# Optimization experiments

Hardware: AMD Instinct MI355X
Metric: run time of the kernel (lower is better)

## Reference

```python
import jax, jax.numpy as jnp
import numpy as np

B, T, E, H = 32, 2048, 512, 512


def setup_inputs() -> dict:
    key = jax.random.key(0)
    k1, k2, k3 = jax.random.split(key, 3)
    scale_w = 1.0 / np.sqrt(E)
    scale_u = 1.0 / np.sqrt(H)
    return {
        "src_seq": jax.random.normal(k1, (B, T, E), dtype=jnp.float32),
        "W": jax.random.normal(k2, (E, 4 * H), dtype=jnp.float32) * scale_w,
        "U": jax.random.normal(k3, (H, 4 * H), dtype=jnp.float32) * scale_u,
        "b": jnp.zeros((4 * H,), dtype=jnp.float32),
        "h0": jnp.zeros((B, H), dtype=jnp.float32),
        "c0": jnp.zeros((B, H), dtype=jnp.float32),
    }


def reference(src_seq, W, U, b, h0, c0):
    """LSTM encoder: scan an LSTMCell over time.

    Returns (output, encoding_hidden_states [T,B,H], final_state), where
    output == final hidden state, matching the original forward().
    """

    def step(carry, x_t):
        h, c = carry
        # Fused gate pre-activations: [B, 4H], keras LSTMCell order i,f,g,o
        z = x_t @ W + h @ U + b
        i, f, g, o = jnp.split(z, 4, axis=-1)
        i = jax.nn.sigmoid(i)
        f = jax.nn.sigmoid(f)
        g = jnp.tanh(g)
        o = jax.nn.sigmoid(o)
        c_new = f * c + i * g
        h_new = o * jnp.tanh(c_new)
        return (h_new, c_new), h_new

    xs = jnp.swapaxes(src_seq, 0, 1)  # [T, B, E]
    (h_T, c_T), hs = jax.lax.scan(step, (h0, c0), xs)
    # (output, list-of-per-step hidden states stacked, final hidden state)
    return h_T, hs, h_T
```

## Files before the change

kernel.cpp:

```cpp
#include <hip/hip_runtime.h>
#include <stdint.h>

#define T_STEPS 2048
#define BATCH 32
#define EDIM 512
#define HDIM 512

typedef __attribute__((ext_vector_type(8))) short bf16x8;
typedef __attribute__((ext_vector_type(4))) float f32x4;
typedef unsigned long long u64t;

#define FIXED_WS 0x831000ull

__device__ inline unsigned short f2bf(float x){
    unsigned u = __float_as_uint(x);
    unsigned r = (u + 0x7fffu + ((u >> 16) & 1u)) >> 16;
    return (unsigned short)r;
}
__device__ inline float bf2f(unsigned short s){
    return __uint_as_float(((unsigned)s) << 16);
}
__device__ inline float sigmoid_f(float x){
    return __builtin_amdgcn_rcpf(1.f + __expf(-x));
}
__device__ inline float tanh_f(float x){
    float xc = fminf(30.f, fmaxf(-30.f, x));
    float e = __expf(2.f * xc);
    return (e - 1.f) * __builtin_amdgcn_rcpf(e + 1.f);
}

__global__ void prep_kernel(const float* __restrict__ W, const float* __restrict__ U,
                            const float* __restrict__ h0,
                            unsigned short* __restrict__ Wh, unsigned short* __restrict__ Wl,
                            unsigned short* __restrict__ Uh, unsigned short* __restrict__ Ul,
                            unsigned* __restrict__ hbuf){
    int idx = blockIdx.x * blockDim.x + threadIdx.x;
    int stride = gridDim.x * blockDim.x;
    const int total = 2 * EDIM * 2048;
    for (int i = idx; i < total; i += stride){
        int mat = i >> 20;
        int r = i & 1048575;
        int k = r >> 11;
        int col = r & 2047;
        float v = (mat ? U : W)[(size_t)k * 2048 + col];
        unsigned short hi = f2bf(v);
        unsigned short lo = f2bf(v - bf2f(hi));
        int cg = (col & 511) >> 4;
        int hc = col & 15;
        int g  = col >> 9;
        int kb = k >> 5;
        int kgrp = (k >> 3) & 3;
        int j = k & 7;
        size_t dst = (size_t)cg * 32768 + (size_t)kb * 2048 + (size_t)g * 512
                   + (size_t)(kgrp * 16 + hc) * 8 + j;
        if (mat){ Uh[dst] = hi; Ul[dst] = lo; } else { Wh[dst] = hi; Wl[dst] = lo; }
    }
    for (int i = idx; i < BATCH * HDIM; i += stride){
        float v = h0[i];
        unsigned short hi = f2bf(v);
        unsigned short lo = f2bf(v - bf2f(hi));
        hbuf[i] = (unsigned)hi | ((unsigned)lo << 16);
    }
}

__global__ __launch_bounds__(256) void xw_gemm_chunk(
        const float* __restrict__ src,
        const unsigned short* __restrict__ Wh, const unsigned short* __restrict__ Wl,
        float* __restrict__ xWc, int t0){
    const int bid = blockIdx.x;
    const int mtile = bid >> 5;
    const int cg = bid & 31;
    const int tid = threadIdx.x;
    const int lane = tid & 63;
    const int w = tid >> 6;
    const int tc = mtile * 4 + w;
    const int t = t0 + tc;
    const int lc = lane & 15;
    const int kgrp = lane >> 4;

    const uint4* WhF = reinterpret_cast<const uint4*>(Wh) + (size_t)cg * 4096;
    const uint4* WlF = reinterpret_cast<const uint4*>(Wl) + (size_t)cg * 4096;

    f32x4 acc[2][4];
    #pragma unroll
    for (int bt = 0; bt < 2; bt++)
        #pragma unroll
        for (int ct = 0; ct < 4; ct++)
            #pragma unroll
            for (int r = 0; r < 4; r++) acc[bt][ct][r] = 0.f;

    for (int kb = 0; kb < 16; kb++){
        bf16x8 ah[2], al[2];
        #pragma unroll
        for (int bt = 0; bt < 2; bt++){
            const float* xp = src + ((size_t)(bt * 16 + lc) * 2048 + t) * 512 + kb * 32 + kgrp * 8;
            float xv[8];
            *reinterpret_cast<float4*>(&xv[0]) = *reinterpret_cast<const float4*>(xp);
            *reinterpret_cast<float4*>(&xv[4]) = *reinterpret_cast<const float4*>(xp + 4);
            #pragma unroll
            for (int j = 0; j < 8; j++){
                unsigned short hi = f2bf(xv[j]);
                ah[bt][j] = (short)hi;
                al[bt][j] = (short)f2bf(xv[j] - bf2f(hi));
            }
        }
        #pragma unroll
        for (int ct = 0; ct < 4; ct++){
            uint4 bh4 = WhF[kb * 256 + ct * 64 + lane];
            uint4 bl4 = WlF[kb * 256 + ct * 64 + lane];
            bf16x8 bh = *reinterpret_cast<bf16x8*>(&bh4);
            bf16x8 bl = *reinterpret_cast<bf16x8*>(&bl4);
            #pragma unroll
            for (int bt = 0; bt < 2; bt++){
                acc[bt][ct] = __builtin_amdgcn_mfma_f32_16x16x32_bf16(ah[bt], bh, acc[bt][ct], 0, 0, 0);
                acc[bt][ct] = __builtin_amdgcn_mfma_f32_16x16x32_bf16(ah[bt], bl, acc[bt][ct], 0, 0, 0);
                acc[bt][ct] = __builtin_amdgcn_mfma_f32_16x16x32_bf16(al[bt], bh, acc[bt][ct], 0, 0, 0);
            }
        }
    }
    #pragma unroll
    for (int bt = 0; bt < 2; bt++)
        #pragma unroll
        for (int ct = 0; ct < 4; ct++)
            #pragma unroll
            for (int r = 0; r < 4; r++){
                int row_b = bt * 16 + kgrp * 4 + r;
                xWc[((size_t)tc * 32 + row_b) * 2048 + ct * 512 + cg * 16 + lc] = acc[bt][ct][r];
            }
}

__global__ __launch_bounds__(512, 1) void lstm_scan_fast(
        const float* __restrict__ bias, const float* __restrict__ c0,
        const unsigned short* __restrict__ Uh, const unsigned short* __restrict__ Ul,
        unsigned* __restrict__ hbuf, unsigned* __restrict__ done,
        const float* __restrict__ xWc, float* __restrict__ c_ws,
        float* __restrict__ out, int t0, int tlen){
    const int tid  = threadIdx.x;
    const int cg   = blockIdx.x;
    const int lane = tid & 63;
    const int w    = tid >> 6;
    const int bt   = w >> 2;
    const int kq   = w & 3;
    const int lc   = lane & 15;
    const int kgrp = lane >> 4;
    const int row  = bt * 16 + lc;

    __shared__ float z_lds[4][BATCH][65];

    const int cb  = tid >> 4;
    const int chc = tid & 15;
    const int col = cg * 16 + chc;
    float c_state = (t0 == 0) ? c0[(size_t)cb * HDIM + col] : c_ws[(size_t)cb * HDIM + col];
    float bias_g[4];
    #pragma unroll
    for (int g = 0; g < 4; g++) bias_g[g] = bias[g * HDIM + col];

    const uint4* UhF = reinterpret_cast<const uint4*>(Uh) + (size_t)cg * 4096;
    const uint4* UlF = reinterpret_cast<const uint4*>(Ul) + (size_t)cg * 4096;
    bf16x8 ufh[4][4], ufl[4][4];
    #pragma unroll
    for (int i = 0; i < 4; i++){
        int kb = kq * 4 + i;
        #pragma unroll
        for (int ct = 0; ct < 4; ct++){
            uint4 a  = UhF[kb * 256 + ct * 64 + lane];
            uint4 b2 = UlF[kb * 256 + ct * 64 + lane];
            ufh[i][ct] = *reinterpret_cast<bf16x8*>(&a);
            ufl[i][ct] = *reinterpret_cast<bf16x8*>(&b2);
        }
    }

    f32x4 acc[4];
    #pragma unroll
    for (int ct = 0; ct < 4; ct++)
        #pragma unroll
        for (int r = 0; r < 4; r++) acc[ct][r] = 0.f;

    for (int t = t0; t < t0 + tlen; t++){
        const float* xwp = xWc + ((size_t)(t - t0) * 32 + cb) * 2048 + col;
        float zx0 = xwp[0], zx1 = xwp[512], zx2 = xwp[1024], zx3 = xwp[1536];

        if (t > 0){
            const unsigned tgt = (unsigned)t;
            while (true){
                unsigned f = __hip_atomic_load(&done[lane & 31],
                                               __ATOMIC_RELAXED, __HIP_MEMORY_SCOPE_AGENT);
                if (__all(f >= tgt)) break;
                __builtin_amdgcn_s_sleep(1);
            }
        }

        const u64t* hp = reinterpret_cast<const u64t*>(hbuf)
                       + (size_t)(t & 1) * 8192 + (size_t)row * 256;
        u64t hv[16];
        #pragma unroll
        for (int i = 0; i < 4; i++){
            int base = (kq * 4 + i) * 16 + kgrp * 4;
            #pragma unroll
            for (int jp = 0; jp < 4; jp++)
                hv[i * 4 + jp] = __hip_atomic_load(hp + base + jp,
                                                   __ATOMIC_RELAXED, __HIP_MEMORY_SCOPE_AGENT);
        }

        #pragma unroll
        for (int i = 0; i < 4; i++){
            bf16x8 ah, al;
            #pragma unroll
            for (int jp = 0; jp < 4; jp++){
                u64t q = hv[i * 4 + jp];
                unsigned a = (unsigned)q;
                unsigned b = (unsigned)(q >> 32);
                ah[jp * 2    ] = (short)(a & 0xffffu); al[jp * 2    ] = (short)(a >> 16);
                ah[jp * 2 + 1] = (short)(b & 0xffffu); al[jp * 2 + 1] = (short)(b >> 16);
            }
            #pragma unroll
            for (int ct = 0; ct < 4; ct++){
                acc[ct] = __builtin_amdgcn_mfma_f32_16x16x32_bf16(ah, ufh[i][ct], acc[ct], 0, 0, 0);
                acc[ct] = __builtin_amdgcn_mfma_f32_16x16x32_bf16(ah, ufl[i][ct], acc[ct], 0, 0, 0);
                acc[ct] = __builtin_amdgcn_mfma_f32_16x16x32_bf16(al, ufh[i][ct], acc[ct], 0, 0, 0);
            }
        }

        #pragma unroll
        for (int ct = 0; ct < 4; ct++)
            #pragma unroll
            for (int r = 0; r < 4; r++)
                z_lds[kq][bt * 16 + kgrp * 4 + r][ct * 16 + lc] = acc[ct][r];
        __syncthreads();

        float hn;
        {
            float z0 = z_lds[0][cb][chc]      + z_lds[1][cb][chc]      + z_lds[2][cb][chc]      + z_lds[3][cb][chc]      + zx0 + bias_g[0];
            float z1 = z_lds[0][cb][16 + chc] + z_lds[1][cb][16 + chc] + z_lds[2][cb][16 + chc] + z_lds[3][cb][16 + chc] + zx1 + bias_g[1];
            float z2 = z_lds[0][cb][32 + chc] + z_lds[1][cb][32 + chc] + z_lds[2][cb][32 + chc] + z_lds[3][cb][32 + chc] + zx2 + bias_g[2];
            float z3 = z_lds[0][cb][48 + chc] + z_lds[1][cb][48 + chc] + z_lds[2][cb][48 + chc] + z_lds[3][cb][48 + chc] + zx3 + bias_g[3];
            float ig = sigmoid_f(z0);
            float fg = sigmoid_f(z1);
            float gg = tanh_f(z2);
            float og = sigmoid_f(z3);
            float cn = fg * c_state + ig * gg;
            c_state = cn;
            hn = og * tanh_f(cn);
            unsigned short hi = f2bf(hn);
            unsigned short lo = f2bf(hn - bf2f(hi));
            __hip_atomic_store(&hbuf[(size_t)((t + 1) & 1) * (BATCH * HDIM) + (size_t)cb * HDIM + col],
                               (unsigned)hi | ((unsigned)lo << 16),
                               __ATOMIC_RELAXED, __HIP_MEMORY_SCOPE_AGENT);
        }
        __syncthreads();
        if (tid == 0)
            __hip_atomic_store(&done[cg], (unsigned)(t + 1),
                               __ATOMIC_RELAXED, __HIP_MEMORY_SCOPE_AGENT);

        out[16384 + ((size_t)t * BATCH + cb) * HDIM + col] = hn;
        if (t == T_STEPS - 1){
            out[(size_t)cb * HDIM + col] = hn;
            out[16384 + (size_t)T_STEPS * BATCH * HDIM + (size_t)cb * HDIM + col] = hn;
        }

        #pragma unroll
        for (int ct = 0; ct < 4; ct++)
            #pragma unroll
            for (int r = 0; r < 4; r++) acc[ct][r] = 0.f;
    }
    c_ws[(size_t)cb * HDIM + col] = c_state;
}

__global__ __launch_bounds__(512, 2) void lstm_scan_r7(
        const float* __restrict__ src, const float* __restrict__ bias,
        const float* __restrict__ c0,
        const unsigned short* __restrict__ Wh, const unsigned short* __restrict__ Wl,
        const unsigned short* __restrict__ Uh, const unsigned short* __restrict__ Ul,
        unsigned* __restrict__ hbuf, unsigned* __restrict__ cnt,
        float* __restrict__ out){
    const int tid  = threadIdx.x;
    const int cg   = blockIdx.x;
    const int lane = tid & 63;
    const int w    = tid >> 6;
    const int bt   = w >> 2;
    const int kq   = w & 3;
    const int lc   = lane & 15;
    const int kgrp = lane >> 4;
    const int row  = bt * 16 + lc;

    __shared__ float z_lds[4][BATCH][65];

    const int cb  = tid >> 4;
    const int chc = tid & 15;
    const int col = cg * 16 + chc;
    float c_state = c0[(size_t)cb * HDIM + col];
    float bias_g[4];
    #pragma unroll
    for (int g = 0; g < 4; g++) bias_g[g] = bias[g * HDIM + col];

    const uint4* WhF = reinterpret_cast<const uint4*>(Wh) + (size_t)cg * 4096;
    const uint4* WlF = reinterpret_cast<const uint4*>(Wl) + (size_t)cg * 4096;
    const uint4* UhF = reinterpret_cast<const uint4*>(Uh) + (size_t)cg * 4096;
    const uint4* UlF = reinterpret_cast<const uint4*>(Ul) + (size_t)cg * 4096;

    f32x4 acc[4];
    #pragma unroll
    for (int ct = 0; ct < 4; ct++)
        #pragma unroll
        for (int r = 0; r < 4; r++) acc[ct][r] = 0.f;

    auto phaseA = [&](int t){
        #pragma unroll
        for (int i = 0; i < 4; i++){
            int kb = kq * 4 + i;
            const float* xp = src + ((size_t)row * T_STEPS + t) * EDIM + kb * 32 + kgrp * 8;
            float xv[8];
            *reinterpret_cast<float4*>(&xv[0]) = *reinterpret_cast<const float4*>(xp);
            *reinterpret_cast<float4*>(&xv[4]) = *reinterpret_cast<const float4*>(xp + 4);
            bf16x8 ah, al;
            #pragma unroll
            for (int j = 0; j < 8; j++){
                unsigned short hi = f2bf(xv[j]);
                ah[j] = (short)hi;
                al[j] = (short)f2bf(xv[j] - bf2f(hi));
            }
            #pragma unroll
            for (int ct = 0; ct < 4; ct++){
                uint4 bh4 = WhF[kb * 256 + ct * 64 + lane];
                uint4 bl4 = WlF[kb * 256 + ct * 64 + lane];
                bf16x8 bh = *reinterpret_cast<bf16x8*>(&bh4);
                bf16x8 bl = *reinterpret_cast<bf16x8*>(&bl4);
                acc[ct] = __builtin_amdgcn_mfma_f32_16x16x32_bf16(ah, bh, acc[ct], 0, 0, 0);
                acc[ct] = __builtin_amdgcn_mfma_f32_16x16x32_bf16(ah, bl, acc[ct], 0, 0, 0);
                acc[ct] = __builtin_amdgcn_mfma_f32_16x16x32_bf16(al, bh, acc[ct], 0, 0, 0);
            }
        }
    };

    phaseA(0);

    for (int t = 0; t < T_STEPS; t++){
        if (t > 0){
            if (w == 0){
                const unsigned need = 32u * (unsigned)((t + 1) >> 1);
                while (__hip_atomic_load(&cnt[t & 1], __ATOMIC_RELAXED, __HIP_MEMORY_SCOPE_AGENT) < need)
                    __builtin_amdgcn_s_sleep(1);
            }
            __syncthreads();
        }

        const u64t* hp = reinterpret_cast<const u64t*>(hbuf)
                       + (size_t)(t & 1) * 8192 + (size_t)row * 256;
        u64t hv[16];
        #pragma unroll
        for (int i = 0; i < 4; i++){
            int base = (kq * 4 + i) * 16 + kgrp * 4;
            #pragma unroll
            for (int jp = 0; jp < 4; jp++)
                hv[i * 4 + jp] = __hip_atomic_load(hp + base + jp,
                                                   __ATOMIC_RELAXED, __HIP_MEMORY_SCOPE_AGENT);
        }

        #pragma unroll
        for (int i = 0; i < 4; i++){
            int kb = kq * 4 + i;
            bf16x8 ah, al;
            #pragma unroll
            for (int jp = 0; jp < 4; jp++){
                u64t q = hv[i * 4 + jp];
                unsigned a = (unsigned)q;
                unsigned b = (unsigned)(q >> 32);
                ah[jp * 2    ] = (short)(a & 0xffffu); al[jp * 2    ] = (short)(a >> 16);
                ah[jp * 2 + 1] = (short)(b & 0xffffu); al[jp * 2 + 1] = (short)(b >> 16);
            }
            #pragma unroll
            for (int ct = 0; ct < 4; ct++){
                uint4 uh4 = UhF[kb * 256 + ct * 64 + lane];
                uint4 ul4 = UlF[kb * 256 + ct * 64 + lane];
                bf16x8 uh = *reinterpret_cast<bf16x8*>(&uh4);
                bf16x8 ul = *reinterpret_cast<bf16x8*>(&ul4);
                acc[ct] = __builtin_amdgcn_mfma_f32_16x16x32_bf16(ah, uh, acc[ct], 0, 0, 0);
                acc[ct] = __builtin_amdgcn_mfma_f32_16x16x32_bf16(ah, ul, acc[ct], 0, 0, 0);
                acc[ct] = __builtin_amdgcn_mfma_f32_16x16x32_bf16(al, uh, acc[ct], 0, 0, 0);
            }
        }

        #pragma unroll
        for (int ct = 0; ct < 4; ct++)
            #pragma unroll
            for (int r = 0; r < 4; r++)
                z_lds[kq][bt * 16 + kgrp * 4 + r][ct * 16 + lc] = acc[ct][r];
        __syncthreads();

        {
            float z[4];
            #pragma unroll
            for (int g = 0; g < 4; g++)
                z[g] = z_lds[0][cb][g * 16 + chc] + z_lds[1][cb][g * 16 + chc]
                     + z_lds[2][cb][g * 16 + chc] + z_lds[3][cb][g * 16 + chc] + bias_g[g];
            float ig = 1.f / (1.f + __expf(-z[0]));
            float fg = 1.f / (1.f + __expf(-z[1]));
            float gg = tanhf(z[2]);
            float og = 1.f / (1.f + __expf(-z[3]));
            float cn = fg * c_state + ig * gg;
            c_state = cn;
            float hn = og * tanhf(cn);
            out[16384 + ((size_t)t * BATCH + cb) * HDIM + col] = hn;
            if (t == T_STEPS - 1){
                out[(size_t)cb * HDIM + col] = hn;
                out[16384 + (size_t)T_STEPS * BATCH * HDIM + (size_t)cb * HDIM + col] = hn;
            }
            unsigned short hi = f2bf(hn);
            unsigned short lo = f2bf(hn - bf2f(hi));
            __hip_atomic_store(&hbuf[(size_t)((t + 1) & 1) * (BATCH * HDIM) + (size_t)cb * HDIM + col],
                               (unsigned)hi | ((unsigned)lo << 16),
                               __ATOMIC_RELAXED, __HIP_MEMORY_SCOPE_AGENT);
        }
        __syncthreads();
        if (tid == 0)
            __hip_atomic_fetch_add(&cnt[(t + 1) & 1], 1u,
                                   __ATOMIC_RELAXED, __HIP_MEMORY_SCOPE_AGENT);

        #pragma unroll
        for (int ct = 0; ct < 4; ct++)
            #pragma unroll
            for (int r = 0; r < 4; r++) acc[ct][r] = 0.f;
        if (t + 1 < T_STEPS) phaseA(t + 1);
    }
}

extern "C" void kernel_launch(void* const* d_in, const int* in_sizes, int n_in,
                              void* d_out, int out_size, void* d_ws, size_t ws_size,
                              hipStream_t stream){
    const float* src = (const float*)d_in[0];
    const float* W   = (const float*)d_in[1];
    const float* U   = (const float*)d_in[2];
    const float* b   = (const float*)d_in[3];
    const float* h0  = (const float*)d_in[4];
    const float* c0  = (const float*)d_in[5];
    float* out = (float*)d_out;
    char* ws = (char*)d_ws;

    int TCH = 0;
    const int cand[5] = {256, 128, 64, 32, 16};
    for (int i = 0; i < 5; i++){
        if (FIXED_WS + (size_t)cand[i] * 262144ull <= ws_size){ TCH = cand[i]; break; }
    }

    if (TCH > 0){
        unsigned*       hbuf = (unsigned*)(ws);
        unsigned*       done = (unsigned*)(ws + 0x020000ull);
        float*          c_ws = (float*)(ws + 0x021000ull);
        unsigned short* Wh   = (unsigned short*)(ws + 0x031000ull);
        unsigned short* Wl   = (unsigned short*)(ws + 0x231000ull);
        unsigned short* Uh   = (unsigned short*)(ws + 0x431000ull);
        unsigned short* Ul   = (unsigned short*)(ws + 0x631000ull);
        float*          xWc  = (float*)(ws + FIXED_WS);

        hipMemsetAsync(done, 0, 128, stream);
        prep_kernel<<<1024, 256, 0, stream>>>(W, U, h0, Wh, Wl, Uh, Ul, hbuf);
        const int nch = T_STEPS / TCH;
        for (int i = 0; i < nch; i++){
            int t0 = i * TCH;
            xw_gemm_chunk<<<(TCH / 4) * 32, 256, 0, stream>>>(src, Wh, Wl, xWc, t0);
            lstm_scan_fast<<<32, 512, 0, stream>>>(b, c0, Uh, Ul, hbuf, done,
                                                   xWc, c_ws, out, t0, TCH);
        }
    } else {
        unsigned*       hbuf = (unsigned*)(ws);
        unsigned*       cnt  = (unsigned*)(ws + 0x20000);
        unsigned short* Wh   = (unsigned short*)(ws + 0x21000);
        unsigned short* Wl   = Wh + 1048576;
        unsigned short* Uh   = Wl + 1048576;
        unsigned short* Ul   = Uh + 1048576;
        hipMemsetAsync(cnt, 0, 8, stream);
        prep_kernel<<<1024, 256, 0, stream>>>(W, U, h0, Wh, Wl, Uh, Ul, hbuf);
        lstm_scan_r7<<<32, 512, 0, stream>>>(src, b, c0, Wh, Wl, Uh, Ul, hbuf, cnt, out);
    }
}
```

Measured before the change: 11.71 ms.

## Replace per-block done flags with step-tagged hidden-state words for sync

Each hidden-state element is now stored as a 64-bit word that carries the step index in its upper half. Consumers poll their own h words directly and start MFMAs on verified groups while later groups are still loading, instead of waiting on a separate done-flag array. This drops the extra __syncthreads and flag store per step, and also raises the chunk-size candidates so there are fewer xW GEMM/scan launch pairs. The cost is twice the h-buffer traffic, and the spin loop gives up after 4096 tries, which could silently consume stale data.

```diff
diff --git a/kernel.cpp b/kernel.cpp
--- a/kernel.cpp
+++ b/kernel.cpp
@@ -10,7 +10,13 @@
 typedef __attribute__((ext_vector_type(4))) float f32x4;
 typedef unsigned long long u64t;
 
-#define FIXED_WS 0x831000ull
+#define OFF_HBUF  0x000000ull
+#define OFF_CWS   0x040000ull
+#define OFF_WH    0x051000ull
+#define OFF_WL    0x251000ull
+#define OFF_UH    0x451000ull
+#define OFF_UL    0x651000ull
+#define FIXED_WS  0x851000ull
 
 __device__ inline unsigned short f2bf(float x){
     unsigned u = __float_as_uint(x);
@@ -33,7 +39,7 @@
                             const float* __restrict__ h0,
                             unsigned short* __restrict__ Wh, unsigned short* __restrict__ Wl,
                             unsigned short* __restrict__ Uh, unsigned short* __restrict__ Ul,
-                            unsigned* __restrict__ hbuf){
+                            u64t* __restrict__ hbuf){
     int idx = blockIdx.x * blockDim.x + threadIdx.x;
     int stride = gridDim.x * blockDim.x;
     const int total = 2 * EDIM * 2048;
@@ -56,10 +62,14 @@
         if (mat){ Uh[dst] = hi; Ul[dst] = lo; } else { Wh[dst] = hi; Wl[dst] = lo; }
     }
     for (int i = idx; i < BATCH * HDIM; i += stride){
+        int b = i >> 9;
+        int k = i & 511;
         float v = h0[i];
         unsigned short hi = f2bf(v);
         unsigned short lo = f2bf(v - bf2f(hi));
-        hbuf[i] = (unsigned)hi | ((unsigned)lo << 16);
+        u64t pv = (u64t)((unsigned)hi | ((unsigned)lo << 16));
+        hbuf[(size_t)b * 512 + k] = pv;
+        hbuf[16384 + (size_t)b * 512 + k] = 0x8000000000000000ull;
     }
 }
 
@@ -129,12 +139,11 @@
             }
 }
 
-__global__ __launch_bounds__(512, 1) void lstm_scan_fast(
+__global__ __launch_bounds__(512, 1) void lstm_scan_tag(
         const float* __restrict__ bias, const float* __restrict__ c0,
         const unsigned short* __restrict__ Uh, const unsigned short* __restrict__ Ul,
-        unsigned* __restrict__ hbuf, unsigned* __restrict__ done,
-        const float* __restrict__ xWc, float* __restrict__ c_ws,
-        float* __restrict__ out, int t0, int tlen){
+        u64t* __restrict__ hbuf, const float* __restrict__ xWc,
+        float* __restrict__ c_ws, float* __restrict__ out, int t0, int tlen){
     const int tid  = threadIdx.x;
     const int cg   = blockIdx.x;
     const int lane = tid & 63;
@@ -180,53 +189,66 @@
         const float* xwp = xWc + ((size_t)(t - t0) * 32 + cb) * 2048 + col;
         float zx0 = xwp[0], zx1 = xwp[512], zx2 = xwp[1024], zx3 = xwp[1536];
 
-        if (t > 0){
-            const unsigned tgt = (unsigned)t;
-            while (true){
-                unsigned f = __hip_atomic_load(&done[lane & 31],
-                                               __ATOMIC_RELAXED, __HIP_MEMORY_SCOPE_AGENT);
-                if (__all(f >= tgt)) break;
-                __builtin_amdgcn_s_sleep(1);
-            }
-        }
-
-        const u64t* hp = reinterpret_cast<const u64t*>(hbuf)
-                       + (size_t)(t & 1) * 8192 + (size_t)row * 256;
-        u64t hv[16];
-        #pragma unroll
-        for (int i = 0; i < 4; i++){
-            int base = (kq * 4 + i) * 16 + kgrp * 4;
-            #pragma unroll
-            for (int jp = 0; jp < 4; jp++)
-                hv[i * 4 + jp] = __hip_atomic_load(hp + base + jp,
-                                                   __ATOMIC_RELAXED, __HIP_MEMORY_SCOPE_AGENT);
-        }
-
-        #pragma unroll
-        for (int i = 0; i < 4; i++){
-            bf16x8 ah, al;
-            #pragma unroll
-            for (int jp = 0; jp < 4; jp++){
-                u64t q = hv[i * 4 + jp];
-                unsigned a = (unsigned)q;
-                unsigned b = (unsigned)(q >> 32);
-                ah[jp * 2    ] = (short)(a & 0xffffu); al[jp * 2    ] = (short)(a >> 16);
-                ah[jp * 2 + 1] = (short)(b & 0xffffu); al[jp * 2 + 1] = (short)(b >> 16);
-            }
-            #pragma unroll
-            for (int ct = 0; ct < 4; ct++){
-                acc[ct] = __builtin_amdgcn_mfma_f32_16x16x32_bf16(ah, ufh[i][ct], acc[ct], 0, 0, 0);
-                acc[ct] = __builtin_amdgcn_mfma_f32_16x16x32_bf16(ah, ufl[i][ct], acc[ct], 0, 0, 0);
-                acc[ct] = __builtin_amdgcn_mfma_f32_16x16x32_bf16(al, ufh[i][ct], acc[ct], 0, 0, 0);
-            }
-        }
+        const u64t* hp = hbuf + (size_t)(t & 1) * 16384 + (size_t)row * 512 + kq * 128;
+        const unsigned tg = (unsigned)t;
+        u64t g0[8], g1[8], g2[8], g3[8];
+
+#define ISSUE(G, gi)                                                              \
+        _Pragma("unroll")                                                         \
+        for (int j = 0; j < 8; j++)                                               \
+            G[j] = __hip_atomic_load(hp + (gi) * 32 + kgrp * 8 + j,               \
+                                     __ATOMIC_RELAXED, __HIP_MEMORY_SCOPE_AGENT);
+
+#define VERIFY(G, gi)                                                             \
+        {                                                                         \
+            int spins = 0;                                                        \
+            while (true){                                                         \
+                bool ok = true;                                                   \
+                _Pragma("unroll")                                                 \
+                for (int j = 0; j < 8; j++)                                       \
+                    ok = ok && ((unsigned)(G[j] >> 32) == tg);                    \
+                if (__all(ok)) break;                                             \
+                if (++spins > 4096) break;    \
+                __builtin_amdgcn_s_sleep(1);                                      \
+                ISSUE(G, gi);                                                     \
+            }                                                                     \
+        }
+
+#define MFGRP(G, gi)                                                              \
+        {                                                                         \
+            bf16x8 ah, al;                                                        \
+            _Pragma("unroll")                                                     \
+            for (int j = 0; j < 8; j++){                                          \
+                unsigned p = (unsigned)G[j];                                      \
+                ah[j] = (short)(p & 0xffffu);                                     \
+                al[j] = (short)(p >> 16);                                         \
+            }                                                                     \
+            _Pragma("unroll")                                                     \
+            for (int ct = 0; ct < 4; ct++){                                       \
+                acc[ct] = __builtin_amdgcn_mfma_f32_16x16x32_bf16(ah, ufh[gi][ct], acc[ct], 0, 0, 0); \
+                acc[ct] = __builtin_amdgcn_mfma_f32_16x16x32_bf16(ah, ufl[gi][ct], acc[ct], 0, 0, 0); \
+                acc[ct] = __builtin_amdgcn_mfma_f32_16x16x32_bf16(al, ufh[gi][ct], acc[ct], 0, 0, 0); \
+            }                                                                     \
+        }
+
+        ISSUE(g0, 0); ISSUE(g1, 1);
+        VERIFY(g0, 0); ISSUE(g2, 2); MFGRP(g0, 0);
+        VERIFY(g1, 1); ISSUE(g3, 3); MFGRP(g1, 1);
+        VERIFY(g2, 2); MFGRP(g2, 2);
+        VERIFY(g3, 3); MFGRP(g3, 3);
+
+#undef ISSUE
+#undef VERIFY
+#undef MFGRP
 
         #pragma unroll
         for (int ct = 0; ct < 4; ct++)
             #pragma unroll
             for (int r = 0; r < 4; r++)
                 z_lds[kq][bt * 16 + kgrp * 4 + r][ct * 16 + lc] = acc[ct][r];
-        __syncthreads();
+        asm volatile("s_waitcnt lgkmcnt(0)" ::: "memory");
+        __builtin_amdgcn_s_barrier();
+        __builtin_amdgcn_sched_barrier(0);
 
         float hn;
         {
@@ -243,14 +265,11 @@
             hn = og * tanh_f(cn);
             unsigned short hi = f2bf(hn);
             unsigned short lo = f2bf(hn - bf2f(hi));
-            __hip_atomic_store(&hbuf[(size_t)((t + 1) & 1) * (BATCH * HDIM) + (size_t)cb * HDIM + col],
-                               (unsigned)hi | ((unsigned)lo << 16),
-                               __ATOMIC_RELAXED, __HIP_MEMORY_SCOPE_AGENT);
-        }
-        __syncthreads();
-        if (tid == 0)
-            __hip_atomic_store(&done[cg], (unsigned)(t + 1),
-                               __ATOMIC_RELAXED, __HIP_MEMORY_SCOPE_AGENT);
+            u64t pv = ((u64t)(unsigned)(t + 1) << 32)
+                    | (u64t)((unsigned)hi | ((unsigned)lo << 16));
+            __hip_atomic_store(&hbuf[(size_t)((t + 1) & 1) * 16384 + (size_t)cb * 512 + col],
+                               pv, __ATOMIC_RELAXED, __HIP_MEMORY_SCOPE_AGENT);
+        }
 
         out[16384 + ((size_t)t * BATCH + cb) * HDIM + col] = hn;
         if (t == T_STEPS - 1){
@@ -258,12 +277,50 @@
             out[16384 + (size_t)T_STEPS * BATCH * HDIM + (size_t)cb * HDIM + col] = hn;
         }
 
+        asm volatile("s_waitcnt lgkmcnt(0)" ::: "memory");
+        __builtin_amdgcn_s_barrier();
+        __builtin_amdgcn_sched_barrier(0);
+
         #pragma unroll
         for (int ct = 0; ct < 4; ct++)
             #pragma unroll
             for (int r = 0; r < 4; r++) acc[ct][r] = 0.f;
     }
     c_ws[(size_t)cb * HDIM + col] = c_state;
+}
+
+__global__ void prep_r7(const float* __restrict__ W, const float* __restrict__ U,
+                        const float* __restrict__ h0,
+                        unsigned short* __restrict__ Wh, unsigned short* __restrict__ Wl,
+                        unsigned short* __restrict__ Uh, unsigned short* __restrict__ Ul,
+                        unsigned* __restrict__ hbuf){
+    int idx = blockIdx.x * blockDim.x + threadIdx.x;
+    int stride = gridDim.x * blockDim.x;
+    const int total = 2 * EDIM * 2048;
+    for (int i = idx; i < total; i += stride){
+        int mat = i >> 20;
+        int r = i & 1048575;
+        int k = r >> 11;
+        int col = r & 2047;
+        float v = (mat ? U : W)[(size_t)k * 2048 + col];
+        unsigned short hi = f2bf(v);
+        unsigned short lo = f2bf(v - bf2f(hi));
+        int cg = (col & 511) >> 4;
+        int hc = col & 15;
+        int g  = col >> 9;
+        int kb = k >> 5;
+        int kgrp = (k >> 3) & 3;
+        int j = k & 7;
+        size_t dst = (size_t)cg * 32768 + (size_t)kb * 2048 + (size_t)g * 512
+                   + (size_t)(kgrp * 16 + hc) * 8 + j;
+        if (mat){ Uh[dst] = hi; Ul[dst] = lo; } else { Wh[dst] = hi; Wl[dst] = lo; }
+    }
+    for (int i = idx; i < BATCH * HDIM; i += stride){
+        float v = h0[i];
+        unsigned short hi = f2bf(v);
+        unsigned short lo = f2bf(v - bf2f(hi));
+        hbuf[i] = (unsigned)hi | ((unsigned)lo << 16);
+    }
 }
 
 __global__ __launch_bounds__(512, 2) void lstm_scan_r7(
@@ -437,29 +494,26 @@
     char* ws = (char*)d_ws;
 
     int TCH = 0;
-    const int cand[5] = {256, 128, 64, 32, 16};
-    for (int i = 0; i < 5; i++){
+    const int cand[6] = {1024, 512, 256, 128, 64, 32};
+    for (int i = 0; i < 6; i++){
         if (FIXED_WS + (size_t)cand[i] * 262144ull <= ws_size){ TCH = cand[i]; break; }
     }
 
     if (TCH > 0){
-        unsigned*       hbuf = (unsigned*)(ws);
-        unsigned*       done = (unsigned*)(ws + 0x020000ull);
-        float*          c_ws = (float*)(ws + 0x021000ull);
-        unsigned short* Wh   = (unsigned short*)(ws + 0x031000ull);
-        unsigned short* Wl   = (unsigned short*)(ws + 0x231000ull);
-        unsigned short* Uh   = (unsigned short*)(ws + 0x431000ull);
-        unsigned short* Ul   = (unsigned short*)(ws + 0x631000ull);
+        u64t*           hbuf = (u64t*)(ws + OFF_HBUF);
+        float*          c_ws = (float*)(ws + OFF_CWS);
+        unsigned short* Wh   = (unsigned short*)(ws + OFF_WH);
+        unsigned short* Wl   = (unsigned short*)(ws + OFF_WL);
+        unsigned short* Uh   = (unsigned short*)(ws + OFF_UH);
+        unsigned short* Ul   = (unsigned short*)(ws + OFF_UL);
         float*          xWc  = (float*)(ws + FIXED_WS);
 
-        hipMemsetAsync(done, 0, 128, stream);
         prep_kernel<<<1024, 256, 0, stream>>>(W, U, h0, Wh, Wl, Uh, Ul, hbuf);
         const int nch = T_STEPS / TCH;
         for (int i = 0; i < nch; i++){
             int t0 = i * TCH;
             xw_gemm_chunk<<<(TCH / 4) * 32, 256, 0, stream>>>(src, Wh, Wl, xWc, t0);
-            lstm_scan_fast<<<32, 512, 0, stream>>>(b, c0, Uh, Ul, hbuf, done,
-                                                   xWc, c_ws, out, t0, TCH);
+            lstm_scan_tag<<<32, 512, 0, stream>>>(b, c0, Uh, Ul, hbuf, xWc, c_ws, out, t0, TCH);
         }
     } else {
         unsigned*       hbuf = (unsigned*)(ws);
@@ -469,7 +523,7 @@
         unsigned short* Uh   = Wl + 1048576;
         unsigned short* Ul   = Uh + 1048576;
         hipMemsetAsync(cnt, 0, 8, stream);
-        prep_kernel<<<1024, 256, 0, stream>>>(W, U, h0, Wh, Wl, Uh, Ul, hbuf);
+        prep_r7<<<1024, 256, 0, stream>>>(W, U, h0, Wh, Wl, Uh, Ul, hbuf);
         lstm_scan_r7<<<32, 512, 0, stream>>>(src, b, c0, Wh, Wl, Uh, Ul, hbuf, cnt, out);
     }
 }
```

Measured after the change: 20.25 ms. 1.73x slower.
